# Kernel tuning notes

Measured on AMD Instinct MI355X. Metric: run time of the kernel, lower is better.

The kernel has to match this reference:

```python
import jax, jax.numpy as jnp
import numpy as np

NS, NV = 32, 8                      # scalar / vector multiplicities
N_NODES, N_EDGES, N_EF = 10000, 100000, 64
W1, W2, W3, W4 = NS*NS, NV*NV, NS*NV, NV*NS   # path weight sizes
WNUM = W1 + W2 + W3 + W4            # 1600
D_NODE = NS + 3*NV                  # 56

def mish(x):
    return x * jnp.tanh(jax.nn.softplus(x))

def setup_inputs() -> dict:
    key = jax.random.key(0)
    ks = jax.random.split(key, 8)
    return dict(
        node_attr=jax.random.normal(ks[0], (N_NODES, D_NODE), jnp.float32),
        edge_index=jax.random.randint(ks[1], (2, N_EDGES), 0, N_NODES),
        edge_attr=jax.random.normal(ks[2], (N_EDGES, N_EF), jnp.float32),
        edge_sh=jax.random.normal(ks[3], (N_EDGES, 4), jnp.float32),
        fc1_w=jax.random.normal(ks[4], (N_EF, N_EF), jnp.float32) / np.sqrt(N_EF),
        fc1_b=jnp.zeros((N_EF,), jnp.float32),
        fc2_w=jax.random.normal(ks[5], (N_EF, WNUM), jnp.float32) / np.sqrt(N_EF),
        fc2_b=jnp.zeros((WNUM,), jnp.float32),
        bn_gamma_s=jnp.ones((NS,), jnp.float32),
        bn_beta_s=jnp.zeros((NS,), jnp.float32),
        bn_gamma_v=jnp.ones((NV,), jnp.float32),
    )

def reference(node_attr, edge_index, edge_attr, edge_sh,
              fc1_w, fc1_b, fc2_w, fc2_b,
              bn_gamma_s, bn_beta_s, bn_gamma_v):
    edge_src, edge_dst = edge_index[0], edge_index[1]
    # edge-conditioned TP weights: Linear -> Mish -> Linear
    w = mish(edge_attr @ fc1_w + fc1_b) @ fc2_w + fc2_b            # [E, WNUM]
    w1 = w[:, :W1].reshape(-1, NS, NS)           # 0e x 0e -> 0e
    w2 = w[:, W1:W1+W2].reshape(-1, NV, NV)      # 1o x 0e -> 1o
    w3 = w[:, W1+W2:W1+W2+W3].reshape(-1, NS, NV)  # 0e x 1o -> 1o
    w4 = w[:, W1+W2+W3:].reshape(-1, NV, NS)     # 1o x 1o -> 0e
    # gather destination node features
    x = node_attr[edge_dst]
    s = x[:, :NS]                                # [E,NS]
    v = x[:, NS:].reshape(-1, NV, 3)             # [E,NV,3]
    sh0 = edge_sh[:, 0]                          # [E]
    sh1 = edge_sh[:, 1:4]                        # [E,3]
    # path normalization: 1/sqrt(total fan-in per output irrep) = 1/sqrt(NS+NV)
    a = 1.0 / np.sqrt(float(NS + NV))
    dot = jnp.einsum('euc,ec->eu', v, sh1) / np.sqrt(3.0)  # CG(1,1,0)
    out_s = a * (jnp.einsum('eu,euw->ew', s * sh0[:, None], w1)
               + jnp.einsum('eu,euw->ew', dot, w4))          # [E,NS]
    out_v = a * (jnp.einsum('euc,euw->ewc', v * sh0[:, None, None], w2)
               + jnp.einsum('eu,ec,euw->ewc', s, sh1, w3))   # [E,NV,3]
    tp = jnp.concatenate([out_s, out_v.reshape(-1, 3*NV)], axis=-1)  # [E,D_NODE]
    # scatter-mean over edge_src
    summ = jax.ops.segment_sum(tp, edge_src, num_segments=N_NODES)
    cnt = jax.ops.segment_sum(jnp.ones((N_EDGES,), tp.dtype), edge_src, num_segments=N_NODES)
    out = summ / jnp.maximum(cnt, 1.0)[:, None]
    # residual (in/out irreps equal -> pad is a no-op)
    out = out + node_attr
    # e3nn-style BatchNorm (training batch stats), eps=1e-4, component norm
    eps = 1e-4
    os = out[:, :NS]
    ov = out[:, NS:].reshape(-1, NV, 3)
    mu = os.mean(axis=0)
    osc = os - mu
    var = (osc * osc).mean(axis=0)
    os_n = osc * jax.lax.rsqrt(var + eps) * bn_gamma_s + bn_beta_s
    vn = (ov * ov).mean(axis=-1).mean(axis=0)                 # [NV]
    ov_n = ov * (jax.lax.rsqrt(vn + eps) * bn_gamma_v)[None, :, None]
    return jnp.concatenate([os_n, ov_n.reshape(-1, 3*NV)], axis=-1)
```

## Files before the change

### kernel.cpp

```cpp
#include <hip/hip_runtime.h>
#include <stdint.h>

#define NNODES 10000
#define NEDGES 100000
#define DNODE 56
#define JTOT 1600
#define HBLK 391
#define TBLK 400

typedef __attribute__((ext_vector_type(8))) short short8;
typedef __attribute__((ext_vector_type(4))) float floatx4;

__device__ __forceinline__ unsigned short f2bf(float f) {
  unsigned u = __float_as_uint(f);
  u = u + 0x7fffu + ((u >> 16) & 1u);
  return (unsigned short)(u >> 16);
}

__device__ __forceinline__ float mishf(float x) {
  float e = __expf(x);
  float z = 1.f + e; z = z * z;
  float t = (z - 1.f) / (z + 1.f);
  t = (x > 40.f) ? 1.f : t;
  return x * t;
}

__global__ __launch_bounds__(256) void k_hidtr(const float* __restrict__ ea,
                                               const float* __restrict__ fc1w,
                                               const float* __restrict__ fc1b,
                                               const float* __restrict__ fc2w,
                                               const int* __restrict__ eidx,
                                               int* __restrict__ cntn,
                                               unsigned short* __restrict__ hb,
                                               unsigned short* __restrict__ G) {
  int bid = blockIdx.x;
  if (bid >= HBLK) {
    int idx = (bid - HBLK) * 256 + threadIdx.x;
    if (idx < 64 * JTOT) {
      int j = idx >> 6, k = idx & 63;
      G[idx] = f2bf(fc2w[k * JTOT + j]);
    }
    return;
  }
  int e = bid * 256 + threadIdx.x;
  if (e >= NEDGES) return;
  atomicAdd(&cntn[eidx[e]], 1);
  float a[64];
  const float4* row = (const float4*)(ea + (size_t)e * 64);
  #pragma unroll
  for (int i = 0; i < 16; i++) {
    float4 t = row[i];
    a[4*i] = t.x; a[4*i+1] = t.y; a[4*i+2] = t.z; a[4*i+3] = t.w;
  }
  for (int jb = 0; jb < 64; jb += 8) {
    float acc[8];
    #pragma unroll
    for (int i = 0; i < 8; i++) acc[i] = fc1b[jb + i];
    #pragma unroll
    for (int k = 0; k < 64; k++) {
      #pragma unroll
      for (int i = 0; i < 8; i++) acc[i] = fmaf(a[k], fc1w[k*64 + jb + i], acc[i]);
    }
    unsigned pk[4];
    #pragma unroll
    for (int i = 0; i < 4; i++) {
      unsigned lo = f2bf(mishf(acc[2*i]));
      unsigned hi = f2bf(mishf(acc[2*i+1]));
      pk[i] = lo | (hi << 16);
    }
    *(uint4*)(hb + (size_t)e*64 + jb) = make_uint4(pk[0], pk[1], pk[2], pk[3]);
  }
}

__global__ __launch_bounds__(1024) void k_scan(const int* __restrict__ cntn,
                                               int* __restrict__ offs,
                                               int* __restrict__ cursor) {
  __shared__ int ts[1024];
  int t = threadIdx.x;
  int base = t * 10;
  int loc[10]; int s = 0;
  #pragma unroll
  for (int i = 0; i < 10; i++) {
    int idx = base + i;
    int v = (idx < NNODES) ? cntn[idx] : 0;
    loc[i] = s; s += v;
  }
  ts[t] = s;
  __syncthreads();
  for (int off = 1; off < 1024; off <<= 1) {
    int v = (t >= off) ? ts[t - off] : 0;
    __syncthreads();
    ts[t] += v;
    __syncthreads();
  }
  int excl = (t == 0) ? 0 : ts[t - 1];
  #pragma unroll
  for (int i = 0; i < 10; i++) {
    int idx = base + i;
    if (idx < NNODES) { int o = excl + loc[i]; offs[idx] = o; cursor[idx] = o; }
  }
  if (t == 1023) offs[NNODES] = ts[1023];
}

__global__ __launch_bounds__(256, 3) void k_tp(
    const unsigned short* __restrict__ hb,
    const unsigned short* __restrict__ G,
    const float* __restrict__ fc2b,
    const int* __restrict__ eidx,
    const float* __restrict__ node_attr,
    const float* __restrict__ edge_sh,
    int* __restrict__ cursor,
    float* __restrict__ tp) {
  __shared__ short Gs[2][2][1024];
  __shared__ float b2s[JTOT];
  __shared__ float Wt4[4][64 * 32];
  __shared__ int pos_s[4][32];
  const int tid = threadIdx.x;
  const int wave = tid >> 6, lane = tid & 63;
  for (int i = tid; i < JTOT; i += 256) b2s[i] = fc2b[i];

  const int e0w = blockIdx.x * 128 + wave * 32;
  float* Wt = &Wt4[wave][0];
  {
    int el = lane & 31, hh = lane >> 5;
    int e = e0w + el;
    bool valid = e < NEDGES;
    int dst = valid ? eidx[NEDGES + e] : 0;
    const float* na = node_attr + (size_t)dst * DNODE;
    if (hh == 0) {
      pos_s[wave][el] = valid ? atomicAdd(&cursor[eidx[e]], 1) : 0;
      #pragma unroll
      for (int u = 0; u < 32; u += 4) {
        float4 t = valid ? *(const float4*)(na + u) : make_float4(0.f,0.f,0.f,0.f);
        Wt[(u+0)*32 + el] = t.x;
        Wt[(u+1)*32 + el] = t.y;
        Wt[(u+2)*32 + el] = t.z;
        Wt[(u+3)*32 + el] = t.w;
      }
    } else {
      float4 sh = valid ? *(const float4*)(edge_sh + 4*(size_t)e) : make_float4(0.f,0.f,0.f,0.f);
      const float rs3 = 0.57735026918962576f;
      #pragma unroll
      for (int u = 0; u < 8; u++) {
        float v0 = valid ? na[32 + u*3 + 0] : 0.f;
        float v1 = valid ? na[32 + u*3 + 1] : 0.f;
        float v2 = valid ? na[32 + u*3 + 2] : 0.f;
        Wt[(32 + u*3 + 0)*32 + el] = v0;
        Wt[(32 + u*3 + 1)*32 + el] = v1;
        Wt[(32 + u*3 + 2)*32 + el] = v2;
        Wt[(56 + u)*32 + el] = (v0*sh.y + v1*sh.z + v2*sh.w) * rs3;
      }
    }
  }

  const int col = lane & 15, rg = lane >> 4, rgh = rg >> 1;
  float sh0c[2], sh1c[2][3];
  bool vld[2];
  short8 bfrag[2][2];
  const short8 zfrag = {0,0,0,0,0,0,0,0};
  #pragma unroll
  for (int nt = 0; nt < 2; nt++) {
    int e = e0w + nt*16 + col;
    bool v = e < NEDGES; vld[nt] = v;
    if (v) {
      float4 sh = *(const float4*)(edge_sh + 4*(size_t)e);
      sh0c[nt] = sh.x; sh1c[nt][0] = sh.y; sh1c[nt][1] = sh.z; sh1c[nt][2] = sh.w;
      const unsigned short* hp = hb + (size_t)e * 64;
      bfrag[nt][0] = *(const short8*)(hp + rg*8);
      bfrag[nt][1] = *(const short8*)(hp + 32 + rg*8);
    } else {
      sh0c[nt] = 0.f; sh1c[nt][0] = sh1c[nt][1] = sh1c[nt][2] = 0.f;
      bfrag[nt][0] = zfrag; bfrag[nt][1] = zfrag;
    }
  }

  float sacc[2][8], vacc[2][12];
  #pragma unroll
  for (int nt = 0; nt < 2; nt++) {
    #pragma unroll
    for (int i = 0; i < 8; i++) sacc[nt][i] = 0.f;
    #pragma unroll
    for (int i = 0; i < 12; i++) vacc[nt][i] = 0.f;
  }

  auto stage = [&](int c) {
    int t = tid >> 7, gt = tid & 127;
    int jp = gt >> 3, g = gt & 7;
    int gsw = (gt & ~7) | (g ^ (jp & 7));
    short8 v = *(const short8*)(G + (size_t)c*2048 + tid*8);
    *(short8*)(&Gs[c&1][t][gsw*8]) = v;
  };

  const int g0 = (rg ^ (col & 7)) * 8;
  const int g1 = ((rg + 4) ^ (col & 7)) * 8;

  stage(0);
  __syncthreads();

  #pragma unroll 1
  for (int c = 0; c < 50; c++) {
    if (c < 49) stage(c + 1);
    #pragma unroll
    for (int t = 0; t < 2; t++) {
      const int jt = c*2 + t;
      const short* gb = &Gs[c&1][t][0];
      short8 x0 = *(const short8*)(gb + col*64 + g0);
      short8 x1 = *(const short8*)(gb + col*64 + g1);
      float4 bb = *(const float4*)&b2s[jt*16 + rg*4];
      floatx4 acc[2];
      #pragma unroll
      for (int nt = 0; nt < 2; nt++) {
        floatx4 cc = {bb.x, bb.y, bb.z, bb.w};
        cc = __builtin_amdgcn_mfma_f32_16x16x32_bf16(x0, bfrag[nt][0], cc, 0, 0, 0);
        cc = __builtin_amdgcn_mfma_f32_16x16x32_bf16(x1, bfrag[nt][1], cc, 0, 0, 0);
        acc[nt] = cc;
      }
      if (jt < 64) {
        const int u = jt >> 1, p = jt & 1;
        #pragma unroll
        for (int nt = 0; nt < 2; nt++) {
          float cf = Wt[u*32 + nt*16 + col] * sh0c[nt];
          #pragma unroll
          for (int r = 0; r < 4; r++)
            sacc[nt][p*4+r] = fmaf(cf, acc[nt][r], sacc[nt][p*4+r]);
        }
      } else if (jt < 68) {
        const int u = (jt - 64)*2 + rgh;
        #pragma unroll
        for (int nt = 0; nt < 2; nt++) {
          #pragma unroll
          for (int c3 = 0; c3 < 3; c3++) {
            float cf = Wt[(32 + u*3 + c3)*32 + nt*16 + col] * sh0c[nt];
            #pragma unroll
            for (int r = 0; r < 4; r++)
              vacc[nt][c3*4+r] = fmaf(cf, acc[nt][r], vacc[nt][c3*4+r]);
          }
        }
      } else if (jt < 84) {
        const int u = (jt - 68)*2 + rgh;
        #pragma unroll
        for (int nt = 0; nt < 2; nt++) {
          float sv = Wt[u*32 + nt*16 + col];
          #pragma unroll
          for (int c3 = 0; c3 < 3; c3++) {
            float cf = sv * sh1c[nt][c3];
            #pragma unroll
            for (int r = 0; r < 4; r++)
              vacc[nt][c3*4+r] = fmaf(cf, acc[nt][r], vacc[nt][c3*4+r]);
          }
        }
      } else {
        const int u = (jt - 84) >> 1, p = jt & 1;
        #pragma unroll
        for (int nt = 0; nt < 2; nt++) {
          float cf = Wt[(56 + u)*32 + nt*16 + col];
          #pragma unroll
          for (int r = 0; r < 4; r++)
            sacc[nt][p*4+r] = fmaf(cf, acc[nt][r], sacc[nt][p*4+r]);
        }
      }
    }
    __syncthreads();
  }

  const float ascale = 0.15811388300841897f;
  #pragma unroll
  for (int nt = 0; nt < 2; nt++) {
    int el = nt*16 + col;
    float* rowp = tp + (size_t)pos_s[wave][el] * DNODE;
    if (vld[nt]) {
      #pragma unroll
      for (int p = 0; p < 2; p++) {
        float4 v = make_float4(ascale*sacc[nt][p*4+0], ascale*sacc[nt][p*4+1],
                               ascale*sacc[nt][p*4+2], ascale*sacc[nt][p*4+3]);
        *(float4*)(rowp + p*16 + rg*4) = v;
      }
    }
    float vtot[12];
    #pragma unroll
    for (int k = 0; k < 12; k++)
      vtot[k] = (vacc[nt][k] + __shfl_xor(vacc[nt][k], 32)) * ascale;
    if (rg < 2 && vld[nt]) {
      float tmp[12];
      #pragma unroll
      for (int c3 = 0; c3 < 3; c3++)
        #pragma unroll
        for (int r = 0; r < 4; r++) tmp[r*3 + c3] = vtot[c3*4 + r];
      #pragma unroll
      for (int j = 0; j < 3; j++)
        *(float4*)(rowp + 32 + (rg & 1)*12 + j*4) = *(float4*)&tmp[j*4];
    }
  }
}

__global__ __launch_bounds__(256) void k_gather(const float* __restrict__ tp,
                                                const int* __restrict__ offs,
                                                const float* __restrict__ node_attr,
                                                float* __restrict__ pre,
                                                float* __restrict__ pstat) {
  __shared__ float redS[4*64], redQ[4*64];
  int t = threadIdx.x, wave = t >> 6, lane = t & 63;
  int gw = blockIdx.x * 4 + wave;
  const int W = 640 * 4;
  int off = (lane < DNODE) ? lane : 0;
  float ssum = 0.f, ssq = 0.f;
  for (int n = gw; n < NNODES; n += W) {
    int beg = offs[n], end = offs[n+1];
    float acc = 0.f;
    int i = beg;
    for (; i + 4 <= end; i += 4) {
      float v0 = tp[(size_t)(i+0)*DNODE + off];
      float v1 = tp[(size_t)(i+1)*DNODE + off];
      float v2 = tp[(size_t)(i+2)*DNODE + off];
      float v3 = tp[(size_t)(i+3)*DNODE + off];
      acc += (v0 + v1) + (v2 + v3);
    }
    for (; i < end; i++) acc += tp[(size_t)i*DNODE + off];
    int c = end - beg; if (c < 1) c = 1;
    float m = acc / (float)c + node_attr[(size_t)n*DNODE + off];
    if (lane < DNODE) { pre[(size_t)n*DNODE + lane] = m; ssum += m; ssq += m*m; }
  }
  redS[wave*64 + lane] = ssum;
  redQ[wave*64 + lane] = ssq;
  __syncthreads();
  if (wave == 0 && lane < DNODE) {
    float a = redS[lane] + redS[64+lane] + redS[128+lane] + redS[192+lane];
    float b = redQ[lane] + redQ[64+lane] + redQ[128+lane] + redQ[192+lane];
    pstat[(size_t)blockIdx.x*112 + lane] = a;
    pstat[(size_t)blockIdx.x*112 + 56 + lane] = b;
  }
}

__global__ __launch_bounds__(256) void k_stats(const float* __restrict__ pstat,
                                               float* __restrict__ stats) {
  int f = blockIdx.x * 4 + (threadIdx.x >> 6);
  int lane = threadIdx.x & 63;
  float v = 0.f;
  for (int b = lane; b < 640; b += 64) v += pstat[(size_t)b*112 + f];
  #pragma unroll
  for (int o = 32; o; o >>= 1) v += __shfl_xor(v, o);
  if (lane == 0) stats[f] = v;
}

__global__ __launch_bounds__(256) void k_norm(const float* __restrict__ pre,
                                              const float* __restrict__ stats,
                                              const float* __restrict__ gs,
                                              const float* __restrict__ bs,
                                              const float* __restrict__ gv,
                                              float* __restrict__ out) {
  int idx = blockIdx.x * 256 + threadIdx.x;
  if (idx >= NNODES * DNODE) return;
  int n = idx / DNODE;
  int d = idx - n * DNODE;
  float val = pre[idx];
  const float invN = 1.f / (float)NNODES;
  float res;
  if (d < 32) {
    float mu = stats[d] * invN;
    float var = stats[56 + d] * invN - mu * mu;
    res = (val - mu) * rsqrtf(var + 1e-4f) * gs[d] + bs[d];
  } else {
    int wi = (d - 32) / 3;
    float vn = (stats[56 + 32 + wi*3] + stats[56 + 32 + wi*3 + 1] +
                stats[56 + 32 + wi*3 + 2]) * (invN / 3.f);
    res = val * rsqrtf(vn + 1e-4f) * gv[wi];
  }
  out[idx] = res;
}

extern "C" void kernel_launch(void* const* d_in, const int* in_sizes, int n_in,
                              void* d_out, int out_size, void* d_ws, size_t ws_size,
                              hipStream_t stream) {
  const float* node_attr = (const float*)d_in[0];
  const int*   eidx      = (const int*)d_in[1];
  const float* edge_attr = (const float*)d_in[2];
  const float* edge_sh   = (const float*)d_in[3];
  const float* fc1w      = (const float*)d_in[4];
  const float* fc1b      = (const float*)d_in[5];
  const float* fc2w      = (const float*)d_in[6];
  const float* fc2b      = (const float*)d_in[7];
  const float* gs        = (const float*)d_in[8];
  const float* bs        = (const float*)d_in[9];
  const float* gv        = (const float*)d_in[10];

  float* ws = (float*)d_ws;
  float* tp    = ws;
  float* pre   = ws + 5600000;
  float* stats = ws + 6160000;
  float* pstat = ws + 6160128;
  int*   cntn  = (int*)(ws + 6231808);
  int*   offs  = (int*)(ws + 6241808);
  int*   cursor= (int*)(ws + 6251816);
  unsigned short* G  = (unsigned short*)(ws + 6261816);
  unsigned short* hb = (unsigned short*)(ws + 6313016);

  hipMemsetAsync(cntn, 0, (size_t)10000 * 4, stream);
  k_hidtr<<<HBLK + TBLK, 256, 0, stream>>>(edge_attr, fc1w, fc1b, fc2w, eidx, cntn, hb, G);
  k_scan<<<1, 1024, 0, stream>>>(cntn, offs, cursor);
  k_tp<<<782, 256, 0, stream>>>(hb, G, fc2b, eidx, node_attr, edge_sh, cursor, tp);
  k_gather<<<640, 256, 0, stream>>>(tp, offs, node_attr, pre, pstat);
  k_stats<<<28, 256, 0, stream>>>(pstat, stats);
  k_norm<<<(NNODES * DNODE + 255) / 256, 256, 0, stream>>>(pre, stats, gs, bs, gv, (float*)d_out);
}
```

Baseline: 241.3 us.

## Load fc2 weight fragments directly from global, drop LDS staging and per-chunk barriers

The tensor-product kernel no longer stages fc2 weight tiles into shared memory behind per-chunk __syncthreads. Each wave loads its MFMA A-fragments straight from global (L2-resident) into registers, prefetching the next pair. Node features in LDS are stored as bf16 and blocks shrink to 128 threads to allow higher occupancy. The scan is rewritten as a single-wave shuffle scan. The cost is more redundant global/L2 traffic per wave, plus bf16 rounding of the node-feature coefficients, which may affect accuracy.

```diff
diff --git a/kernel.cpp b/kernel.cpp
--- a/kernel.cpp
+++ b/kernel.cpp
@@ -15,6 +15,9 @@
   unsigned u = __float_as_uint(f);
   u = u + 0x7fffu + ((u >> 16) & 1u);
   return (unsigned short)(u >> 16);
+}
+__device__ __forceinline__ float bf2f(unsigned short u) {
+  return __uint_as_float(((unsigned)u) << 16);
 }
 
 __device__ __forceinline__ float mishf(float x) {
@@ -72,37 +75,35 @@
   }
 }
 
-__global__ __launch_bounds__(1024) void k_scan(const int* __restrict__ cntn,
-                                               int* __restrict__ offs,
-                                               int* __restrict__ cursor) {
-  __shared__ int ts[1024];
-  int t = threadIdx.x;
-  int base = t * 10;
-  int loc[10]; int s = 0;
-  #pragma unroll
-  for (int i = 0; i < 10; i++) {
+__global__ __launch_bounds__(64) void k_scan(const int* __restrict__ cntn,
+                                             int* __restrict__ offs,
+                                             int* __restrict__ cursor) {
+  const int PER = 157;
+  int lane = threadIdx.x;
+  int base = lane * PER;
+  int s = 0;
+  for (int i = 0; i < PER; i++) {
     int idx = base + i;
-    int v = (idx < NNODES) ? cntn[idx] : 0;
-    loc[i] = s; s += v;
-  }
-  ts[t] = s;
-  __syncthreads();
-  for (int off = 1; off < 1024; off <<= 1) {
-    int v = (t >= off) ? ts[t - off] : 0;
-    __syncthreads();
-    ts[t] += v;
-    __syncthreads();
-  }
-  int excl = (t == 0) ? 0 : ts[t - 1];
-  #pragma unroll
-  for (int i = 0; i < 10; i++) {
+    if (idx < NNODES) s += cntn[idx];
+  }
+  int incl = s;
+  #pragma unroll
+  for (int o = 1; o < 64; o <<= 1) {
+    int v = __shfl_up(incl, o);
+    if (lane >= o) incl += v;
+  }
+  int run = incl - s;
+  for (int i = 0; i < PER; i++) {
     int idx = base + i;
-    if (idx < NNODES) { int o = excl + loc[i]; offs[idx] = o; cursor[idx] = o; }
-  }
-  if (t == 1023) offs[NNODES] = ts[1023];
-}
-
-__global__ __launch_bounds__(256, 3) void k_tp(
+    if (idx < NNODES) {
+      offs[idx] = run; cursor[idx] = run;
+      run += cntn[idx];
+    }
+  }
+  if (lane == 63) offs[NNODES] = run;
+}
+
+__global__ __launch_bounds__(128, 4) void k_tp(
     const unsigned short* __restrict__ hb,
     const unsigned short* __restrict__ G,
     const float* __restrict__ fc2b,
@@ -111,16 +112,15 @@
     const float* __restrict__ edge_sh,
     int* __restrict__ cursor,
     float* __restrict__ tp) {
-  __shared__ short Gs[2][2][1024];
   __shared__ float b2s[JTOT];
-  __shared__ float Wt4[4][64 * 32];
-  __shared__ int pos_s[4][32];
+  __shared__ unsigned short wls[2][64 * 32];
+  __shared__ int pos_s[2][32];
   const int tid = threadIdx.x;
   const int wave = tid >> 6, lane = tid & 63;
-  for (int i = tid; i < JTOT; i += 256) b2s[i] = fc2b[i];
-
-  const int e0w = blockIdx.x * 128 + wave * 32;
-  float* Wt = &Wt4[wave][0];
+  for (int i = tid; i < JTOT; i += 128) b2s[i] = fc2b[i];
+
+  const int e0w = blockIdx.x * 64 + wave * 32;
+  unsigned short* Wt = &wls[wave][0];
   {
     int el = lane & 31, hh = lane >> 5;
     int e = e0w + el;
@@ -132,10 +132,10 @@
       #pragma unroll
       for (int u = 0; u < 32; u += 4) {
         float4 t = valid ? *(const float4*)(na + u) : make_float4(0.f,0.f,0.f,0.f);
-        Wt[(u+0)*32 + el] = t.x;
-        Wt[(u+1)*32 + el] = t.y;
-        Wt[(u+2)*32 + el] = t.z;
-        Wt[(u+3)*32 + el] = t.w;
+        Wt[(u+0)*32 + el] = f2bf(t.x);
+        Wt[(u+1)*32 + el] = f2bf(t.y);
+        Wt[(u+2)*32 + el] = f2bf(t.z);
+        Wt[(u+3)*32 + el] = f2bf(t.w);
       }
     } else {
       float4 sh = valid ? *(const float4*)(edge_sh + 4*(size_t)e) : make_float4(0.f,0.f,0.f,0.f);
@@ -145,13 +145,14 @@
         float v0 = valid ? na[32 + u*3 + 0] : 0.f;
         float v1 = valid ? na[32 + u*3 + 1] : 0.f;
         float v2 = valid ? na[32 + u*3 + 2] : 0.f;
-        Wt[(32 + u*3 + 0)*32 + el] = v0;
-        Wt[(32 + u*3 + 1)*32 + el] = v1;
-        Wt[(32 + u*3 + 2)*32 + el] = v2;
-        Wt[(56 + u)*32 + el] = (v0*sh.y + v1*sh.z + v2*sh.w) * rs3;
-      }
-    }
-  }
+        Wt[(32 + u*3 + 0)*32 + el] = f2bf(v0);
+        Wt[(32 + u*3 + 1)*32 + el] = f2bf(v1);
+        Wt[(32 + u*3 + 2)*32 + el] = f2bf(v2);
+        Wt[(56 + u)*32 + el] = f2bf((v0*sh.y + v1*sh.z + v2*sh.w) * rs3);
+      }
+    }
+  }
+  __syncthreads();
 
   const int col = lane & 15, rg = lane >> 4, rgh = rg >> 1;
   float sh0c[2], sh1c[2][3];
@@ -183,84 +184,90 @@
     for (int i = 0; i < 12; i++) vacc[nt][i] = 0.f;
   }
 
-  auto stage = [&](int c) {
-    int t = tid >> 7, gt = tid & 127;
-    int jp = gt >> 3, g = gt & 7;
-    int gsw = (gt & ~7) | (g ^ (jp & 7));
-    short8 v = *(const short8*)(G + (size_t)c*2048 + tid*8);
-    *(short8*)(&Gs[c&1][t][gsw*8]) = v;
+  auto ldpair = [&](int pp, short8& f0, short8& f1, short8& f2, short8& f3) {
+    const unsigned short* q = G + (((pp*32) + col) << 6) + rg*8;
+    f0 = *(const short8*)q;
+    f1 = *(const short8*)(q + 32);
+    f2 = *(const short8*)(q + 1024);
+    f3 = *(const short8*)(q + 1024 + 32);
   };
 
-  const int g0 = (rg ^ (col & 7)) * 8;
-  const int g1 = ((rg + 4) ^ (col & 7)) * 8;
-
-  stage(0);
-  __syncthreads();
+  short8 c0, c1, c2, c3, n0, n1, n2, n3;
+  ldpair(0, c0, c1, c2, c3);
 
   #pragma unroll 1
-  for (int c = 0; c < 50; c++) {
-    if (c < 49) stage(c + 1);
-    #pragma unroll
-    for (int t = 0; t < 2; t++) {
-      const int jt = c*2 + t;
-      const short* gb = &Gs[c&1][t][0];
-      short8 x0 = *(const short8*)(gb + col*64 + g0);
-      short8 x1 = *(const short8*)(gb + col*64 + g1);
-      float4 bb = *(const float4*)&b2s[jt*16 + rg*4];
-      floatx4 acc[2];
+  for (int pp = 0; pp < 50; pp++) {
+    if (pp < 49) ldpair(pp + 1, n0, n1, n2, n3);
+    const int jt0 = 2*pp;
+    float4 bb0 = *(const float4*)&b2s[jt0*16 + rg*4];
+    float4 bb1 = *(const float4*)&b2s[(jt0+1)*16 + rg*4];
+    floatx4 acc0[2], acc1[2];
+    #pragma unroll
+    for (int nt = 0; nt < 2; nt++) {
+      floatx4 a0 = {bb0.x, bb0.y, bb0.z, bb0.w};
+      a0 = __builtin_amdgcn_mfma_f32_16x16x32_bf16(c0, bfrag[nt][0], a0, 0, 0, 0);
+      a0 = __builtin_amdgcn_mfma_f32_16x16x32_bf16(c1, bfrag[nt][1], a0, 0, 0, 0);
+      acc0[nt] = a0;
+      floatx4 a1 = {bb1.x, bb1.y, bb1.z, bb1.w};
+      a1 = __builtin_amdgcn_mfma_f32_16x16x32_bf16(c2, bfrag[nt][0], a1, 0, 0, 0);
+      a1 = __builtin_amdgcn_mfma_f32_16x16x32_bf16(c3, bfrag[nt][1], a1, 0, 0, 0);
+      acc1[nt] = a1;
+    }
+    if (pp < 32) {
       #pragma unroll
       for (int nt = 0; nt < 2; nt++) {
-        floatx4 cc = {bb.x, bb.y, bb.z, bb.w};
-        cc = __builtin_amdgcn_mfma_f32_16x16x32_bf16(x0, bfrag[nt][0], cc, 0, 0, 0);
-        cc = __builtin_amdgcn_mfma_f32_16x16x32_bf16(x1, bfrag[nt][1], cc, 0, 0, 0);
-        acc[nt] = cc;
-      }
-      if (jt < 64) {
-        const int u = jt >> 1, p = jt & 1;
+        float cf = bf2f(Wt[pp*32 + nt*16 + col]) * sh0c[nt];
         #pragma unroll
-        for (int nt = 0; nt < 2; nt++) {
-          float cf = Wt[u*32 + nt*16 + col] * sh0c[nt];
+        for (int r = 0; r < 4; r++) {
+          sacc[nt][r]   = fmaf(cf, acc0[nt][r], sacc[nt][r]);
+          sacc[nt][4+r] = fmaf(cf, acc1[nt][r], sacc[nt][4+r]);
+        }
+      }
+    } else if (pp < 34) {
+      const int u0 = (jt0 - 64)*2 + rgh, u1 = u0 + 2;
+      #pragma unroll
+      for (int nt = 0; nt < 2; nt++) {
+        #pragma unroll
+        for (int q = 0; q < 3; q++) {
+          float cf0 = bf2f(Wt[(32 + u0*3 + q)*32 + nt*16 + col]) * sh0c[nt];
+          float cf1 = bf2f(Wt[(32 + u1*3 + q)*32 + nt*16 + col]) * sh0c[nt];
           #pragma unroll
-          for (int r = 0; r < 4; r++)
-            sacc[nt][p*4+r] = fmaf(cf, acc[nt][r], sacc[nt][p*4+r]);
-        }
-      } else if (jt < 68) {
-        const int u = (jt - 64)*2 + rgh;
-        #pragma unroll
-        for (int nt = 0; nt < 2; nt++) {
-          #pragma unroll
-          for (int c3 = 0; c3 < 3; c3++) {
-            float cf = Wt[(32 + u*3 + c3)*32 + nt*16 + col] * sh0c[nt];
-            #pragma unroll
-            for (int r = 0; r < 4; r++)
-              vacc[nt][c3*4+r] = fmaf(cf, acc[nt][r], vacc[nt][c3*4+r]);
+          for (int r = 0; r < 4; r++) {
+            vacc[nt][q*4+r] = fmaf(cf0, acc0[nt][r], vacc[nt][q*4+r]);
+            vacc[nt][q*4+r] = fmaf(cf1, acc1[nt][r], vacc[nt][q*4+r]);
           }
         }
-      } else if (jt < 84) {
-        const int u = (jt - 68)*2 + rgh;
+      }
+    } else if (pp < 42) {
+      const int u0 = (jt0 - 68)*2 + rgh, u1 = u0 + 2;
+      #pragma unroll
+      for (int nt = 0; nt < 2; nt++) {
+        float sv0 = bf2f(Wt[u0*32 + nt*16 + col]);
+        float sv1 = bf2f(Wt[u1*32 + nt*16 + col]);
         #pragma unroll
-        for (int nt = 0; nt < 2; nt++) {
-          float sv = Wt[u*32 + nt*16 + col];
+        for (int q = 0; q < 3; q++) {
+          float cf0 = sv0 * sh1c[nt][q];
+          float cf1 = sv1 * sh1c[nt][q];
           #pragma unroll
-          for (int c3 = 0; c3 < 3; c3++) {
-            float cf = sv * sh1c[nt][c3];
-            #pragma unroll
-            for (int r = 0; r < 4; r++)
-              vacc[nt][c3*4+r] = fmaf(cf, acc[nt][r], vacc[nt][c3*4+r]);
+          for (int r = 0; r < 4; r++) {
+            vacc[nt][q*4+r] = fmaf(cf0, acc0[nt][r], vacc[nt][q*4+r]);
+            vacc[nt][q*4+r] = fmaf(cf1, acc1[nt][r], vacc[nt][q*4+r]);
           }
         }
-      } else {
-        const int u = (jt - 84) >> 1, p = jt & 1;
+      }
+    } else {
+      const int u = pp - 42;
+      #pragma unroll
+      for (int nt = 0; nt < 2; nt++) {
+        float cf = bf2f(Wt[(56 + u)*32 + nt*16 + col]);
         #pragma unroll
-        for (int nt = 0; nt < 2; nt++) {
-          float cf = Wt[(56 + u)*32 + nt*16 + col];
-          #pragma unroll
-          for (int r = 0; r < 4; r++)
-            sacc[nt][p*4+r] = fmaf(cf, acc[nt][r], sacc[nt][p*4+r]);
+        for (int r = 0; r < 4; r++) {
+          sacc[nt][r]   = fmaf(cf, acc0[nt][r], sacc[nt][r]);
+          sacc[nt][4+r] = fmaf(cf, acc1[nt][r], sacc[nt][4+r]);
         }
       }
     }
-    __syncthreads();
+    c0 = n0; c1 = n1; c2 = n2; c3 = n3;
   }
 
   const float ascale = 0.15811388300841897f;
@@ -283,9 +290,9 @@
     if (rg < 2 && vld[nt]) {
       float tmp[12];
       #pragma unroll
-      for (int c3 = 0; c3 < 3; c3++)
+      for (int q = 0; q < 3; q++)
         #pragma unroll
-        for (int r = 0; r < 4; r++) tmp[r*3 + c3] = vtot[c3*4 + r];
+        for (int r = 0; r < 4; r++) tmp[r*3 + q] = vtot[q*4 + r];
       #pragma unroll
       for (int j = 0; j < 3; j++)
         *(float4*)(rowp + 32 + (rg & 1)*12 + j*4) = *(float4*)&tmp[j*4];
@@ -396,8 +403,8 @@
 
   hipMemsetAsync(cntn, 0, (size_t)10000 * 4, stream);
   k_hidtr<<<HBLK + TBLK, 256, 0, stream>>>(edge_attr, fc1w, fc1b, fc2w, eidx, cntn, hb, G);
-  k_scan<<<1, 1024, 0, stream>>>(cntn, offs, cursor);
-  k_tp<<<782, 256, 0, stream>>>(hb, G, fc2b, eidx, node_attr, edge_sh, cursor, tp);
+  k_scan<<<1, 64, 0, stream>>>(cntn, offs, cursor);
+  k_tp<<<1563, 128, 0, stream>>>(hb, G, fc2b, eidx, node_attr, edge_sh, cursor, tp);
   k_gather<<<640, 256, 0, stream>>>(tp, offs, node_attr, pre, pstat);
   k_stats<<<28, 256, 0, stream>>>(pstat, stats);
   k_norm<<<(NNODES * DNODE + 255) / 256, 256, 0, stream>>>(pre, stats, gs, bs, gv, (float*)d_out);
```

New measurement: 455.5 us. +88.8%, slower.

## Fold scan and stats into last-block epilogues, async-load larger G chunks

Applied to the files above, without the earlier changes.

Moves the prefix scan into the last finishing block of the hidden-layer kernel and the stats reduction into the last block of the gather kernel, using atomic done counters. This removes two kernel launches. The tp kernel now stages 10 jt tiles per chunk with global_load_lds async copies, and G is pre-swizzled in the transpose kernel. Each block starts at a rotated chunk to spread L2 traffic, and per-edge node features in LDS are stored as bf16 to save LDS. The risks are a serialized single-block scan tail, reduced occupancy (launch bounds drop from 3 to 2 blocks) and extra bf16 rounding of node features.

```diff
diff --git a/kernel.cpp b/kernel.cpp
--- a/kernel.cpp
+++ b/kernel.cpp
@@ -16,6 +16,9 @@
   u = u + 0x7fffu + ((u >> 16) & 1u);
   return (unsigned short)(u >> 16);
 }
+__device__ __forceinline__ float bf2f(unsigned short u) {
+  return __uint_as_float(((unsigned)u) << 16);
+}
 
 __device__ __forceinline__ float mishf(float x) {
   float e = __expf(x);
@@ -25,84 +28,101 @@
   return x * t;
 }
 
+__device__ __forceinline__ void async_ld16(void* lds, const void* gp) {
+  __builtin_amdgcn_global_load_lds(
+      (const __attribute__((address_space(1))) unsigned int*)gp,
+      (__attribute__((address_space(3))) unsigned int*)lds, 16, 0, 0);
+}
+
 __global__ __launch_bounds__(256) void k_hidtr(const float* __restrict__ ea,
                                                const float* __restrict__ fc1w,
                                                const float* __restrict__ fc1b,
                                                const float* __restrict__ fc2w,
                                                const int* __restrict__ eidx,
                                                int* __restrict__ cntn,
+                                               int* __restrict__ done,
+                                               int* __restrict__ offs,
+                                               int* __restrict__ cursor,
                                                unsigned short* __restrict__ hb,
                                                unsigned short* __restrict__ G) {
-  int bid = blockIdx.x;
+  __shared__ int ssum[256];
+  __shared__ int amLast;
+  const int bid = blockIdx.x, t = threadIdx.x;
   if (bid >= HBLK) {
-    int idx = (bid - HBLK) * 256 + threadIdx.x;
+    int idx = (bid - HBLK) * 256 + t;
     if (idx < 64 * JTOT) {
-      int j = idx >> 6, k = idx & 63;
+      int jt = idx >> 10, r = idx & 1023;
+      int col = r >> 6, w = r & 63;
+      int slot = w >> 3, s = w & 7;
+      int g = slot ^ (col & 7);
+      int k = g * 8 + s;
+      int j = jt * 16 + col;
       G[idx] = f2bf(fc2w[k * JTOT + j]);
     }
-    return;
-  }
-  int e = bid * 256 + threadIdx.x;
-  if (e >= NEDGES) return;
-  atomicAdd(&cntn[eidx[e]], 1);
-  float a[64];
-  const float4* row = (const float4*)(ea + (size_t)e * 64);
-  #pragma unroll
-  for (int i = 0; i < 16; i++) {
-    float4 t = row[i];
-    a[4*i] = t.x; a[4*i+1] = t.y; a[4*i+2] = t.z; a[4*i+3] = t.w;
-  }
-  for (int jb = 0; jb < 64; jb += 8) {
-    float acc[8];
-    #pragma unroll
-    for (int i = 0; i < 8; i++) acc[i] = fc1b[jb + i];
-    #pragma unroll
-    for (int k = 0; k < 64; k++) {
-      #pragma unroll
-      for (int i = 0; i < 8; i++) acc[i] = fmaf(a[k], fc1w[k*64 + jb + i], acc[i]);
-    }
-    unsigned pk[4];
-    #pragma unroll
-    for (int i = 0; i < 4; i++) {
-      unsigned lo = f2bf(mishf(acc[2*i]));
-      unsigned hi = f2bf(mishf(acc[2*i+1]));
-      pk[i] = lo | (hi << 16);
-    }
-    *(uint4*)(hb + (size_t)e*64 + jb) = make_uint4(pk[0], pk[1], pk[2], pk[3]);
-  }
-}
-
-__global__ __launch_bounds__(1024) void k_scan(const int* __restrict__ cntn,
-                                               int* __restrict__ offs,
-                                               int* __restrict__ cursor) {
-  __shared__ int ts[1024];
-  int t = threadIdx.x;
-  int base = t * 10;
-  int loc[10]; int s = 0;
-  #pragma unroll
-  for (int i = 0; i < 10; i++) {
-    int idx = base + i;
-    int v = (idx < NNODES) ? cntn[idx] : 0;
-    loc[i] = s; s += v;
-  }
-  ts[t] = s;
-  __syncthreads();
-  for (int off = 1; off < 1024; off <<= 1) {
-    int v = (t >= off) ? ts[t - off] : 0;
+  } else {
+    int e = bid * 256 + t;
+    if (e < NEDGES) {
+      atomicAdd(&cntn[eidx[e]], 1);
+      float a[64];
+      const float4* row = (const float4*)(ea + (size_t)e * 64);
+      #pragma unroll
+      for (int i = 0; i < 16; i++) {
+        float4 v = row[i];
+        a[4*i] = v.x; a[4*i+1] = v.y; a[4*i+2] = v.z; a[4*i+3] = v.w;
+      }
+      for (int jb = 0; jb < 64; jb += 8) {
+        float acc[8];
+        #pragma unroll
+        for (int i = 0; i < 8; i++) acc[i] = fc1b[jb + i];
+        #pragma unroll
+        for (int k = 0; k < 64; k++) {
+          #pragma unroll
+          for (int i = 0; i < 8; i++) acc[i] = fmaf(a[k], fc1w[k*64 + jb + i], acc[i]);
+        }
+        unsigned pk[4];
+        #pragma unroll
+        for (int i = 0; i < 4; i++) {
+          unsigned lo = f2bf(mishf(acc[2*i]));
+          unsigned hi = f2bf(mishf(acc[2*i+1]));
+          pk[i] = lo | (hi << 16);
+        }
+        *(uint4*)(hb + (size_t)e*64 + jb) = make_uint4(pk[0], pk[1], pk[2], pk[3]);
+      }
+    }
+  }
+  __syncthreads();
+  if (t == 0) {
+    __threadfence();
+    amLast = (atomicAdd(done, 1) == (HBLK + TBLK) - 1) ? 1 : 0;
+  }
+  __syncthreads();
+  if (amLast) {
+    __threadfence();
+    int c[40]; int s = 0;
+    #pragma unroll 4
+    for (int i = 0; i < 40; i++) {
+      int idx = t*40 + i;
+      int v = (idx < NNODES) ? atomicAdd(&cntn[idx], 0) : 0;
+      c[i] = v; s += v;
+    }
+    ssum[t] = s;
     __syncthreads();
-    ts[t] += v;
-    __syncthreads();
-  }
-  int excl = (t == 0) ? 0 : ts[t - 1];
-  #pragma unroll
-  for (int i = 0; i < 10; i++) {
-    int idx = base + i;
-    if (idx < NNODES) { int o = excl + loc[i]; offs[idx] = o; cursor[idx] = o; }
-  }
-  if (t == 1023) offs[NNODES] = ts[1023];
-}
-
-__global__ __launch_bounds__(256, 3) void k_tp(
+    for (int o = 1; o < 256; o <<= 1) {
+      int v = (t >= o) ? ssum[t - o] : 0;
+      __syncthreads();
+      ssum[t] += v;
+      __syncthreads();
+    }
+    int run = (t == 0) ? 0 : ssum[t - 1];
+    for (int i = 0; i < 40; i++) {
+      int idx = t*40 + i;
+      if (idx < NNODES) { offs[idx] = run; cursor[idx] = run; run += c[i]; }
+    }
+    if (t == 255) offs[NNODES] = ssum[255];
+  }
+}
+
+__global__ __launch_bounds__(256, 2) void k_tp(
     const unsigned short* __restrict__ hb,
     const unsigned short* __restrict__ G,
     const float* __restrict__ fc2b,
@@ -111,16 +131,16 @@
     const float* __restrict__ edge_sh,
     int* __restrict__ cursor,
     float* __restrict__ tp) {
-  __shared__ short Gs[2][2][1024];
+  __shared__ short Gs[2][10 * 1024];
+  __shared__ unsigned short wls[4][64 * 32];
   __shared__ float b2s[JTOT];
-  __shared__ float Wt4[4][64 * 32];
   __shared__ int pos_s[4][32];
   const int tid = threadIdx.x;
   const int wave = tid >> 6, lane = tid & 63;
   for (int i = tid; i < JTOT; i += 256) b2s[i] = fc2b[i];
 
   const int e0w = blockIdx.x * 128 + wave * 32;
-  float* Wt = &Wt4[wave][0];
+  unsigned short* Wt = &wls[wave][0];
   {
     int el = lane & 31, hh = lane >> 5;
     int e = e0w + el;
@@ -131,11 +151,11 @@
       pos_s[wave][el] = valid ? atomicAdd(&cursor[eidx[e]], 1) : 0;
       #pragma unroll
       for (int u = 0; u < 32; u += 4) {
-        float4 t = valid ? *(const float4*)(na + u) : make_float4(0.f,0.f,0.f,0.f);
-        Wt[(u+0)*32 + el] = t.x;
-        Wt[(u+1)*32 + el] = t.y;
-        Wt[(u+2)*32 + el] = t.z;
-        Wt[(u+3)*32 + el] = t.w;
+        float4 v = valid ? *(const float4*)(na + u) : make_float4(0.f,0.f,0.f,0.f);
+        Wt[(u+0)*32 + el] = f2bf(v.x);
+        Wt[(u+1)*32 + el] = f2bf(v.y);
+        Wt[(u+2)*32 + el] = f2bf(v.z);
+        Wt[(u+3)*32 + el] = f2bf(v.w);
       }
     } else {
       float4 sh = valid ? *(const float4*)(edge_sh + 4*(size_t)e) : make_float4(0.f,0.f,0.f,0.f);
@@ -145,15 +165,17 @@
         float v0 = valid ? na[32 + u*3 + 0] : 0.f;
         float v1 = valid ? na[32 + u*3 + 1] : 0.f;
         float v2 = valid ? na[32 + u*3 + 2] : 0.f;
-        Wt[(32 + u*3 + 0)*32 + el] = v0;
-        Wt[(32 + u*3 + 1)*32 + el] = v1;
-        Wt[(32 + u*3 + 2)*32 + el] = v2;
-        Wt[(56 + u)*32 + el] = (v0*sh.y + v1*sh.z + v2*sh.w) * rs3;
+        Wt[(32 + u*3 + 0)*32 + el] = f2bf(v0);
+        Wt[(32 + u*3 + 1)*32 + el] = f2bf(v1);
+        Wt[(32 + u*3 + 2)*32 + el] = f2bf(v2);
+        Wt[(56 + u)*32 + el] = f2bf((v0*sh.y + v1*sh.z + v2*sh.w) * rs3);
       }
     }
   }
 
   const int col = lane & 15, rg = lane >> 4, rgh = rg >> 1;
+  const int g0 = (rg ^ (col & 7)) * 8;
+  const int g1 = ((rg + 4) ^ (col & 7)) * 8;
   float sh0c[2], sh1c[2][3];
   bool vld[2];
   short8 bfrag[2][2];
@@ -183,43 +205,42 @@
     for (int i = 0; i < 12; i++) vacc[nt][i] = 0.f;
   }
 
-  auto stage = [&](int c) {
-    int t = tid >> 7, gt = tid & 127;
-    int jp = gt >> 3, g = gt & 7;
-    int gsw = (gt & ~7) | (g ^ (jp & 7));
-    short8 v = *(const short8*)(G + (size_t)c*2048 + tid*8);
-    *(short8*)(&Gs[c&1][t][gsw*8]) = v;
+  auto stage = [&](int ch, int b) {
+    const unsigned short* gsrc = G + (size_t)ch * 10240 + tid * 8;
+    #pragma unroll
+    for (int i = 0; i < 5; i++)
+      async_ld16(&Gs[b][(i*256 + wave*64) * 8], gsrc + i*256*8);
   };
 
-  const int g0 = (rg ^ (col & 7)) * 8;
-  const int g1 = ((rg + 4) ^ (col & 7)) * 8;
-
-  stage(0);
-  __syncthreads();
-
+  const int cc0 = blockIdx.x % 10;
+  stage(cc0, 0);
+  __syncthreads();
+
+  int buf = 0;
   #pragma unroll 1
-  for (int c = 0; c < 50; c++) {
-    if (c < 49) stage(c + 1);
-    #pragma unroll
-    for (int t = 0; t < 2; t++) {
-      const int jt = c*2 + t;
-      const short* gb = &Gs[c&1][t][0];
+  for (int cc = 0; cc < 10; cc++) {
+    int c = cc0 + cc; if (c >= 10) c -= 10;
+    if (cc < 9) { int cn = c + 1; if (cn >= 10) cn = 0; stage(cn, buf ^ 1); }
+    #pragma unroll 1
+    for (int t = 0; t < 10; t++) {
+      const int jt = c * 10 + t;
+      const short* gb = &Gs[buf][t * 1024];
       short8 x0 = *(const short8*)(gb + col*64 + g0);
       short8 x1 = *(const short8*)(gb + col*64 + g1);
       float4 bb = *(const float4*)&b2s[jt*16 + rg*4];
       floatx4 acc[2];
       #pragma unroll
       for (int nt = 0; nt < 2; nt++) {
-        floatx4 cc = {bb.x, bb.y, bb.z, bb.w};
-        cc = __builtin_amdgcn_mfma_f32_16x16x32_bf16(x0, bfrag[nt][0], cc, 0, 0, 0);
-        cc = __builtin_amdgcn_mfma_f32_16x16x32_bf16(x1, bfrag[nt][1], cc, 0, 0, 0);
-        acc[nt] = cc;
+        floatx4 a = {bb.x, bb.y, bb.z, bb.w};
+        a = __builtin_amdgcn_mfma_f32_16x16x32_bf16(x0, bfrag[nt][0], a, 0, 0, 0);
+        a = __builtin_amdgcn_mfma_f32_16x16x32_bf16(x1, bfrag[nt][1], a, 0, 0, 0);
+        acc[nt] = a;
       }
       if (jt < 64) {
         const int u = jt >> 1, p = jt & 1;
         #pragma unroll
         for (int nt = 0; nt < 2; nt++) {
-          float cf = Wt[u*32 + nt*16 + col] * sh0c[nt];
+          float cf = bf2f(Wt[u*32 + nt*16 + col]) * sh0c[nt];
           #pragma unroll
           for (int r = 0; r < 4; r++)
             sacc[nt][p*4+r] = fmaf(cf, acc[nt][r], sacc[nt][p*4+r]);
@@ -229,37 +250,38 @@
         #pragma unroll
         for (int nt = 0; nt < 2; nt++) {
           #pragma unroll
-          for (int c3 = 0; c3 < 3; c3++) {
-            float cf = Wt[(32 + u*3 + c3)*32 + nt*16 + col] * sh0c[nt];
+          for (int q = 0; q < 3; q++) {
+            float cf = bf2f(Wt[(32 + u*3 + q)*32 + nt*16 + col]) * sh0c[nt];
             #pragma unroll
             for (int r = 0; r < 4; r++)
-              vacc[nt][c3*4+r] = fmaf(cf, acc[nt][r], vacc[nt][c3*4+r]);
+              vacc[nt][q*4+r] = fmaf(cf, acc[nt][r], vacc[nt][q*4+r]);
           }
         }
       } else if (jt < 84) {
         const int u = (jt - 68)*2 + rgh;
         #pragma unroll
         for (int nt = 0; nt < 2; nt++) {
-          float sv = Wt[u*32 + nt*16 + col];
+          float sv = bf2f(Wt[u*32 + nt*16 + col]);
           #pragma unroll
-          for (int c3 = 0; c3 < 3; c3++) {
-            float cf = sv * sh1c[nt][c3];
+          for (int q = 0; q < 3; q++) {
+            float cf = sv * sh1c[nt][q];
             #pragma unroll
             for (int r = 0; r < 4; r++)
-              vacc[nt][c3*4+r] = fmaf(cf, acc[nt][r], vacc[nt][c3*4+r]);
+              vacc[nt][q*4+r] = fmaf(cf, acc[nt][r], vacc[nt][q*4+r]);
           }
         }
       } else {
         const int u = (jt - 84) >> 1, p = jt & 1;
         #pragma unroll
         for (int nt = 0; nt < 2; nt++) {
-          float cf = Wt[(56 + u)*32 + nt*16 + col];
+          float cf = bf2f(Wt[(56 + u)*32 + nt*16 + col]);
           #pragma unroll
           for (int r = 0; r < 4; r++)
             sacc[nt][p*4+r] = fmaf(cf, acc[nt][r], sacc[nt][p*4+r]);
         }
       }
     }
+    buf ^= 1;
     __syncthreads();
   }
 
@@ -283,9 +305,9 @@
     if (rg < 2 && vld[nt]) {
       float tmp[12];
       #pragma unroll
-      for (int c3 = 0; c3 < 3; c3++)
-        #pragma unroll
-        for (int r = 0; r < 4; r++) tmp[r*3 + c3] = vtot[c3*4 + r];
+      for (int q = 0; q < 3; q++)
+        #pragma unroll
+        for (int r = 0; r < 4; r++) tmp[r*3 + q] = vtot[q*4 + r];
       #pragma unroll
       for (int j = 0; j < 3; j++)
         *(float4*)(rowp + 32 + (rg & 1)*12 + j*4) = *(float4*)&tmp[j*4];
@@ -297,8 +319,11 @@
                                                 const int* __restrict__ offs,
                                                 const float* __restrict__ node_attr,
                                                 float* __restrict__ pre,
-                                                float* __restrict__ pstat) {
+                                                float* __restrict__ pstat,
+                                                int* __restrict__ gdone,
+                                                float* __restrict__ stats) {
   __shared__ float redS[4*64], redQ[4*64];
+  __shared__ int amLast;
   int t = threadIdx.x, wave = t >> 6, lane = t & 63;
   int gw = blockIdx.x * 4 + wave;
   const int W = 640 * 4;
@@ -329,17 +354,24 @@
     pstat[(size_t)blockIdx.x*112 + lane] = a;
     pstat[(size_t)blockIdx.x*112 + 56 + lane] = b;
   }
-}
-
-__global__ __launch_bounds__(256) void k_stats(const float* __restrict__ pstat,
-                                               float* __restrict__ stats) {
-  int f = blockIdx.x * 4 + (threadIdx.x >> 6);
-  int lane = threadIdx.x & 63;
-  float v = 0.f;
-  for (int b = lane; b < 640; b += 64) v += pstat[(size_t)b*112 + f];
-  #pragma unroll
-  for (int o = 32; o; o >>= 1) v += __shfl_xor(v, o);
-  if (lane == 0) stats[f] = v;
+  __syncthreads();
+  if (t == 0) {
+    __threadfence();
+    amLast = (atomicAdd(gdone, 1) == 639) ? 1 : 0;
+  }
+  __syncthreads();
+  if (amLast) {
+    __threadfence();
+    int f = t & 127, h = t >> 7;
+    float v = 0.f;
+    if (f < 112) {
+      #pragma unroll 8
+      for (int b = h; b < 640; b += 2) v += pstat[(size_t)b*112 + f];
+      redS[h*128 + f] = v;
+    }
+    __syncthreads();
+    if (t < 112) stats[t] = redS[t] + redS[128 + t];
+  }
 }
 
 __global__ __launch_bounds__(256) void k_norm(const float* __restrict__ pre,
@@ -389,16 +421,17 @@
   float* stats = ws + 6160000;
   float* pstat = ws + 6160128;
   int*   cntn  = (int*)(ws + 6231808);
-  int*   offs  = (int*)(ws + 6241808);
-  int*   cursor= (int*)(ws + 6251816);
-  unsigned short* G  = (unsigned short*)(ws + 6261816);
-  unsigned short* hb = (unsigned short*)(ws + 6313016);
-
-  hipMemsetAsync(cntn, 0, (size_t)10000 * 4, stream);
-  k_hidtr<<<HBLK + TBLK, 256, 0, stream>>>(edge_attr, fc1w, fc1b, fc2w, eidx, cntn, hb, G);
-  k_scan<<<1, 1024, 0, stream>>>(cntn, offs, cursor);
+  int*   done  = (int*)(ws + 6241808);
+  int*   gdone = (int*)(ws + 6241809);
+  int*   offs  = (int*)(ws + 6241824);
+  int*   cursor= (int*)(ws + 6251832);
+  unsigned short* G  = (unsigned short*)(ws + 6271832);
+  unsigned short* hb = (unsigned short*)(ws + 6323032);
+
+  hipMemsetAsync(cntn, 0, (size_t)10002 * 4, stream);
+  k_hidtr<<<HBLK + TBLK, 256, 0, stream>>>(edge_attr, fc1w, fc1b, fc2w, eidx,
+                                           cntn, done, offs, cursor, hb, G);
   k_tp<<<782, 256, 0, stream>>>(hb, G, fc2b, eidx, node_attr, edge_sh, cursor, tp);
-  k_gather<<<640, 256, 0, stream>>>(tp, offs, node_attr, pre, pstat);
-  k_stats<<<28, 256, 0, stream>>>(pstat, stats);
+  k_gather<<<640, 256, 0, stream>>>(tp, offs, node_attr, pre, pstat, gdone, stats);
   k_norm<<<(NNODES * DNODE + 255) / 256, 256, 0, stream>>>(pre, stats, gs, bs, gv, (float*)d_out);
 }
```

Result: slower. 328.9 us (+36.3%).
